# Performance work log

Measured on AMD Instinct MI355X. Metric: run time of the kernel, lower is better.

## Reference

```python
import jax, jax.numpy as jnp
import numpy as np

LAMBDA_COLOR = 0.01
BLUR = 0.01          # geomloss blur
P = 2                # geomloss p
EPS_FINAL = BLUR ** P  # 1e-4
# Note: with scaling=1.2 (>1), geomloss's epsilon_schedule arange is empty, so
# eps_list = [diameter**p, blur**p] -> exactly two annealing stages.


def cost_matrix(x, y, lambda_color):
    # x: [B,N,6], y: [B,M,6]
    cx, col_x = x[..., :3], x[..., 3:]
    cy, col_y = y[..., :3], y[..., 3:]
    max_norm = jnp.max(jnp.linalg.norm(jnp.concatenate([cx, cy], axis=1), axis=-1))
    s = 1.0 / (max_norm + 1e-6)
    cxn, cyn = cx * s, cy * s
    coord = jnp.sum((cxn[:, :, None, :] - cyn[:, None, :, :]) ** 2, axis=-1)  # [B,N,M]
    col_x = jnp.clip(col_x, 0.0, 1.0)
    col_y = jnp.clip(col_y, 0.0, 1.0)
    col = jnp.sum((col_x[:, :, None, :] - col_y[:, None, :, :]) ** 2, axis=-1)
    return jnp.maximum(coord + lambda_color * col, 0.0)


def softmin(eps, C, h):
    # h: [B,M] = log_weights + potential/eps ; C: [B,N,M]
    return -eps * jax.nn.logsumexp(h[:, None, :] - C / eps, axis=2)  # [B,N]


def sinkhorn_distance(x, y, lambda_color):
    B, N, _ = x.shape
    M = y.shape[1]
    a_log = jnp.full((B, N), -np.log(N), dtype=x.dtype)
    b_log = jnp.full((B, M), -np.log(M), dtype=x.dtype)

    C_xy = cost_matrix(x, y, lambda_color)          # [B,N,M]
    C_yx = jnp.swapaxes(C_xy, 1, 2)                 # cost is symmetric in x<->y

    # diameter over raw 6-d features (geomloss max_diameter)
    pts = jnp.concatenate([x.reshape(-1, x.shape[-1]), y.reshape(-1, y.shape[-1])], axis=0)
    diameter = jnp.linalg.norm(pts.max(0) - pts.min(0))
    eps_list = (diameter ** P, jnp.asarray(EPS_FINAL, x.dtype))

    # Sinkhorn loop runs without gradient through the potentials (geomloss semantics)
    Cs_xy = jax.lax.stop_gradient(C_xy)
    Cs_yx = jax.lax.stop_gradient(C_yx)

    eps = eps_list[0]
    f = softmin(eps, Cs_xy, b_log)   # potential on x
    g = softmin(eps, Cs_yx, a_log)   # potential on y
    for eps in eps_list:
        ft = softmin(eps, Cs_xy, b_log + g / eps)
        gt = softmin(eps, Cs_yx, a_log + f / eps)
        f, g = 0.5 * (f + ft), 0.5 * (g + gt)

    # final extrapolation with gradient-carrying cost, detached dual potentials
    eps = eps_list[-1]
    f_new = softmin(eps, C_xy, b_log + jax.lax.stop_gradient(g) / eps)
    g_new = softmin(eps, C_yx, a_log + jax.lax.stop_gradient(f) / eps)

    # <a,f> + <b,g> with uniform weights
    ot = f_new.mean(axis=1) + g_new.mean(axis=1)   # [B]
    return ot.mean() * 10.0


def setup_inputs() -> dict:
    key = jax.random.key(0)
    kx, ky = jax.random.split(key)
    x = jax.random.normal(kx, (4, 4096, 6), dtype=jnp.float32)
    y = jax.random.normal(ky, (4, 4096, 6), dtype=jnp.float32)
    return {"x": x, "y": y}


def reference(x, y):
    return sinkhorn_distance(x, y, LAMBDA_COLOR)
```

## Files before the change

### kernel.cpp

```cpp
#include <hip/hip_runtime.h>

#define B_ 4
#define N_ 4096
#define ROWS (B_ * N_)
#define PTS_TOTAL (2 * ROWS)

#define LOG2E 1.4426950408889634f
#define LN2   0.6931471805599453f
#define EPS1  1e-4f
#define NEG_LOG2M (-12.0f)
#define EPS1LNM 8.317766166719343e-4f
#define ENC_STRIDE 32

typedef _Float16 h2 __attribute__((ext_vector_type(2)));
typedef _Float16 v8h __attribute__((ext_vector_type(8)));
typedef float f32x4 __attribute__((ext_vector_type(4)));

__device__ inline float fexp2(float x) { return __builtin_amdgcn_exp2f(x); }
__device__ inline float flog2(float x) { return __builtin_amdgcn_logf(x); }

__device__ inline unsigned fenc(float f) {
  unsigned u = __float_as_uint(f);
  return (u & 0x80000000u) ? ~u : (u | 0x80000000u);
}
__device__ inline float fdec(unsigned u) {
  return (u & 0x80000000u) ? __uint_as_float(u & 0x7fffffffu)
                           : __uint_as_float(~u);
}
__device__ inline unsigned pkh2(float a, float b) {
  h2 hv; hv.x = (_Float16)a; hv.y = (_Float16)b;
  return __builtin_bit_cast(unsigned, hv);
}
__device__ inline v8h bcv8(uint4 u) { return __builtin_bit_cast(v8h, u); }

__global__ void init_kernel(unsigned* enc, float* MOM) {
  int t = threadIdx.x;
  if (t < 13) enc[t * ENC_STRIDE] = 0u;
  if (t < 512) MOM[t] = 0.0f;
}

__global__ __launch_bounds__(256) void reduce_kernel(
    const float* __restrict__ x, const float* __restrict__ y,
    unsigned* __restrict__ enc) {
  int idx = blockIdx.x * 256 + threadIdx.x;
  bool isx = idx < ROWS;
  const float* p = (isx ? x : y) + (size_t)(isx ? idx : idx - ROWS) * 6;
  float d[6];
#pragma unroll
  for (int k = 0; k < 6; ++k) d[k] = p[k];
  unsigned e[13];
  e[0] = fenc(d[0] * d[0] + d[1] * d[1] + d[2] * d[2]);
#pragma unroll
  for (int k = 0; k < 6; ++k) {
    e[1 + k] = fenc(d[k]);
    e[7 + k] = fenc(-d[k]);
  }
#pragma unroll
  for (int off = 32; off > 0; off >>= 1) {
#pragma unroll
    for (int k = 0; k < 13; ++k) {
      unsigned o = (unsigned)__shfl_xor((int)e[k], off);
      e[k] = e[k] > o ? e[k] : o;
    }
  }
  __shared__ unsigned sh[4][13];
  int wave = threadIdx.x >> 6, lane = threadIdx.x & 63;
  if (lane == 0) {
#pragma unroll
    for (int k = 0; k < 13; ++k) sh[wave][k] = e[k];
  }
  __syncthreads();
  if (threadIdx.x < 13) {
    unsigned v = sh[0][threadIdx.x];
#pragma unroll
    for (int w = 1; w < 4; ++w) v = v > sh[w][threadIdx.x] ? v : sh[w][threadIdx.x];
    atomicMax(&enc[threadIdx.x * ENC_STRIDE], v);
  }
}

__global__ __launch_bounds__(256) void pack_kernel(
    const float* __restrict__ x, const float* __restrict__ y,
    float4* __restrict__ XP, uint4* __restrict__ AREC,
    uint4* __restrict__ BREC, const unsigned* __restrict__ enc,
    float* __restrict__ sc, float* __restrict__ MOM1) {
  int g = blockIdx.x * 256 + threadIdx.x;
  int side = g >> 14, local = g & (ROWS - 1), batch = local >> 12;
  float s = 1.0f / (sqrtf(fdec(enc[0])) + 1e-6f);
  float eps0 = 0.0f;
#pragma unroll
  for (int k = 0; k < 6; ++k) {
    float dd = fdec(enc[(1 + k) * ENC_STRIDE]) + fdec(enc[(7 + k) * ENC_STRIDE]);
    eps0 += dd * dd;
  }
  if (g == 0) sc[0] = eps0;

  const float* p = (side ? y : x) + (size_t)local * 6;
  float v[6];
  v[0] = p[0] * s; v[1] = p[1] * s; v[2] = p[2] * s;
  v[3] = 0.1f * fminf(fmaxf(p[3], 0.0f), 1.0f);
  v[4] = 0.1f * fminf(fmaxf(p[4], 0.0f), 1.0f);
  v[5] = 0.1f * fminf(fmaxf(p[5], 0.0f), 1.0f);
  float q = v[0]*v[0] + v[1]*v[1] + v[2]*v[2] + v[3]*v[3] + v[4]*v[4] + v[5]*v[5];
  XP[(size_t)g * 2]     = make_float4(v[0], v[1], v[2], v[3]);
  XP[(size_t)g * 2 + 1] = make_float4(v[4], v[5], q, 0.0f);
  unsigned w01 = pkh2(v[0], v[1]), w23 = pkh2(v[2], v[3]), w45 = pkh2(v[4], v[5]);
  AREC[g] = (uint4){w01, w23, w45, pkh2(1.0f, 0.0f)};
  BREC[g] = (uint4){w01, w23, w45, 0u};

  float w = fexp2(NEG_LOG2M - q * (LOG2E / eps0));
  float acc[28];
  acc[0] = w;
  int kk = 1;
#pragma unroll
  for (int d = 0; d < 6; ++d) acc[kk++] = w * v[d];
#pragma unroll
  for (int d = 0; d < 6; ++d) {
    float wv = w * v[d];
#pragma unroll
    for (int e = d; e < 6; ++e) acc[kk++] = wv * v[e];
  }
#pragma unroll
  for (int off = 32; off > 0; off >>= 1) {
#pragma unroll
    for (int k = 0; k < 28; ++k) acc[k] += __shfl_xor(acc[k], off);
  }
  __shared__ float sh[4][28];
  int wave = threadIdx.x >> 6, lane = threadIdx.x & 63;
  if (lane == 0) {
#pragma unroll
    for (int k = 0; k < 28; ++k) sh[wave][k] = acc[k];
  }
  __syncthreads();
  if (threadIdx.x < 28) {
    float vv = (sh[0][threadIdx.x] + sh[1][threadIdx.x]) +
               (sh[2][threadIdx.x] + sh[3][threadIdx.x]);
    atomicAdd(&MOM1[(side * 4 + batch) * 32 + threadIdx.x], vv);
  }
}

__device__ inline float taylor_f(const float* __restrict__ M, const float* v,
                                 float q, float eps0) {
  float sc2 = 2.0f * LOG2E / eps0;
  float p[6];
#pragma unroll
  for (int d = 0; d < 6; ++d) p[d] = v[d] * sc2;
  float t1 = 0.0f;
#pragma unroll
  for (int d = 0; d < 6; ++d) t1 += p[d] * M[1 + d];
  float t2 = 0.0f;
  int kk = 7;
#pragma unroll
  for (int d = 0; d < 6; ++d) {
#pragma unroll
    for (int e = d; e < 6; ++e) {
      float coef = (d == e) ? 1.0f : 2.0f;
      t2 += coef * p[d] * p[e] * M[kk];
      kk++;
    }
  }
  float S = M[0] + LN2 * t1 + (0.5f * LN2 * LN2) * t2;
  return q - eps0 * LN2 * flog2(S);
}

__global__ __launch_bounds__(256) void rows1_kernel(
    const float4* __restrict__ XP, const float* __restrict__ MOM1,
    float* __restrict__ MOM2, float* __restrict__ FG1,
    const float* __restrict__ sc) {
  int g = blockIdx.x * 256 + threadIdx.x;
  int side = g >> 14, local = g & (ROWS - 1), batch = local >> 12;
  float eps0 = sc[0];
  float4 a = XP[(size_t)g * 2], b = XP[(size_t)g * 2 + 1];
  float v[6] = {a.x, a.y, a.z, a.w, b.x, b.y};
  float q = b.z;
  const float* M = MOM1 + (((side ^ 1) * 4 + batch) * 32);
  float f1 = taylor_f(M, v, q, eps0);
  FG1[g] = f1;
  float w = fexp2(NEG_LOG2M + (f1 - q) * (LOG2E / eps0));
  float acc[28];
  acc[0] = w;
  int kk = 1;
#pragma unroll
  for (int d = 0; d < 6; ++d) acc[kk++] = w * v[d];
#pragma unroll
  for (int d = 0; d < 6; ++d) {
    float wv = w * v[d];
#pragma unroll
    for (int e = d; e < 6; ++e) acc[kk++] = wv * v[e];
  }
#pragma unroll
  for (int off = 32; off > 0; off >>= 1) {
#pragma unroll
    for (int k = 0; k < 28; ++k) acc[k] += __shfl_xor(acc[k], off);
  }
  __shared__ float sh[4][28];
  int wave = threadIdx.x >> 6, lane = threadIdx.x & 63;
  if (lane == 0) {
#pragma unroll
    for (int k = 0; k < 28; ++k) sh[wave][k] = acc[k];
  }
  __syncthreads();
  if (threadIdx.x < 28) {
    float vv = (sh[0][threadIdx.x] + sh[1][threadIdx.x]) +
               (sh[2][threadIdx.x] + sh[3][threadIdx.x]);
    atomicAdd(&MOM2[(side * 4 + batch) * 32 + threadIdx.x], vv);
  }
}

__global__ __launch_bounds__(256) void rows2_kernel(
    const float4* __restrict__ XP, const float* __restrict__ MOM2,
    const float* __restrict__ FG1, float* __restrict__ FG2,
    unsigned* __restrict__ BRECu, const float* __restrict__ sc) {
  int g = blockIdx.x * 256 + threadIdx.x;
  int side = g >> 14, local = g & (ROWS - 1), batch = local >> 12;
  float eps0 = sc[0];
  float4 a = XP[(size_t)g * 2], b = XP[(size_t)g * 2 + 1];
  float v[6] = {a.x, a.y, a.z, a.w, b.x, b.y};
  float q = b.z;
  const float* M = MOM2 + (((side ^ 1) * 4 + batch) * 32);
  float f_t = taylor_f(M, v, q, eps0);
  float f2v = 0.5f * (FG1[g] + f_t);
  FG2[g] = f2v;
  float hs2 = 0.5f * (f2v - q - EPS1LNM);
  BRECu[4 * g + 3] = pkh2(hs2, 0.0f);
}

__global__ __launch_bounds__(256) void softmax_pair_kernel(
    const uint4* __restrict__ AREC, const uint4* __restrict__ BIN,
    uint4* __restrict__ BOUT, const float* __restrict__ XPf,
    const float* __restrict__ prev, float* __restrict__ part) {
  int t = threadIdx.x;
  int wave = t >> 6, lane = t & 63;
  int l16 = lane & 15;
  bool ld = lane < 16;
  int grow0 = blockIdx.x * 32;
  int side = grow0 >> 14;
  int batch = (grow0 & (ROWS - 1)) >> 12;
  int colrec0 = (side ^ 1) * ROWS + batch * 4096 + wave * 1024;

  uint4 z4 = (uint4){0u, 0u, 0u, 0u};
  uint4 a1u = z4, a2u = z4;
  if (ld) {
    a1u = AREC[grow0 + l16];
    a2u = AREC[grow0 + 16 + l16];
  }
  v8h a1 = bcv8(a1u), a2 = bcv8(a2u);

  f32x4 m2a = {-3.0e38f, -3.0e38f, -3.0e38f, -3.0e38f};
  f32x4 m2b = m2a;
  const f32x4 cz = {0.0f, 0.0f, 0.0f, 0.0f};

#pragma unroll 4
  for (int tt = 0; tt < 64; ++tt) {
    uint4 bu = z4;
    if (ld) bu = BIN[colrec0 + tt * 16 + l16];
    v8h b = bcv8(bu);
    f32x4 d1 = __builtin_amdgcn_mfma_f32_16x16x32_f16(a1, b, cz, 0, 0, 0);
    f32x4 d2 = __builtin_amdgcn_mfma_f32_16x16x32_f16(a2, b, cz, 0, 0, 0);
    m2a = __builtin_elementwise_max(m2a, d1);
    m2b = __builtin_elementwise_max(m2b, d2);
  }

#pragma unroll
  for (int off = 1; off <= 8; off <<= 1) {
#pragma unroll
    for (int r = 0; r < 4; ++r) {
      m2a[r] = fmaxf(m2a[r], __shfl_xor(m2a[r], off));
      m2b[r] = fmaxf(m2b[r], __shfl_xor(m2b[r], off));
    }
  }

  __shared__ float lm[4][32];
  __shared__ float fsh[32];
  if (l16 == 0) {
    int qd = lane >> 4;
#pragma unroll
    for (int r = 0; r < 4; ++r) {
      lm[wave][qd * 4 + r] = m2a[r];
      lm[wave][16 + qd * 4 + r] = m2b[r];
    }
  }
  __syncthreads();
  if (t < 32) {
    int g = grow0 + t;
    float m = fmaxf(fmaxf(lm[0][t], lm[1][t]), fmaxf(lm[2][t], lm[3][t]));
    float q = XPf[(size_t)g * 8 + 6];
    float f_t = q - 2.0f * m;
    float fo = prev ? 0.5f * (prev[g] + f_t) : f_t;
    if (BOUT) {
      float hs = 0.5f * (fo - q - EPS1LNM);
      uint4 ar = AREC[g];
      BOUT[g] = (uint4){ar.x, ar.y, ar.z, pkh2(hs, 0.0f)};
    }
    if (part) {
      fsh[t] = fo;
      __builtin_amdgcn_s_waitcnt(0);
      if (t == 0) {
        float ssum = 0.0f;
#pragma unroll
        for (int k = 0; k < 32; ++k) ssum += fsh[k];
        part[blockIdx.x] = ssum;
      }
    }
  }
}

__global__ __launch_bounds__(256) void final_kernel(
    const float* __restrict__ part, float* __restrict__ out) {
  float acc = 0.0f;
  for (int i = threadIdx.x; i < 1024; i += 256) acc += part[i];
  __shared__ float sh[256];
  sh[threadIdx.x] = acc;
  __syncthreads();
  for (int st = 128; st > 0; st >>= 1) {
    if (threadIdx.x < st) sh[threadIdx.x] += sh[threadIdx.x + st];
    __syncthreads();
  }
  if (threadIdx.x == 0) out[0] = sh[0] * (10.0f / (float)ROWS);
}

extern "C" void kernel_launch(void* const* d_in, const int* in_sizes, int n_in,
                              void* d_out, int out_size, void* d_ws,
                              size_t ws_size, hipStream_t stream) {
  const float* x = (const float*)d_in[0];
  const float* y = (const float*)d_in[1];
  float* out = (float*)d_out;
  float* w = (float*)d_ws;
  unsigned* enc = (unsigned*)d_ws;
  float* sc   = w + 448;
  float* MOM  = w + 512;
  float* MOM1 = MOM;
  float* MOM2 = MOM + 256;
  float* base = w + 1024;
  float4* XP   = (float4*)base;
  uint4* AREC  = (uint4*)(base + 262144);
  uint4* BRECA = (uint4*)(base + 262144 + 131072);
  uint4* BRECB = (uint4*)(base + 262144 + 262144);
  float* FG1   = base + 262144 + 262144 + 131072;
  float* FG2   = FG1 + PTS_TOTAL;
  float* PART  = FG2 + PTS_TOTAL;

  init_kernel<<<1, 512, 0, stream>>>(enc, MOM);
  reduce_kernel<<<PTS_TOTAL / 256, 256, 0, stream>>>(x, y, enc);
  pack_kernel<<<PTS_TOTAL / 256, 256, 0, stream>>>(x, y, XP, AREC, BRECA, enc,
                                                   sc, MOM1);
  rows1_kernel<<<PTS_TOTAL / 256, 256, 0, stream>>>(XP, MOM1, MOM2, FG1, sc);
  rows2_kernel<<<PTS_TOTAL / 256, 256, 0, stream>>>(XP, MOM2, FG1, FG2,
                                                    (unsigned*)BRECA, sc);
  softmax_pair_kernel<<<1024, 256, 0, stream>>>(AREC, BRECA, BRECB,
                                                (const float*)XP, FG2, nullptr);
  softmax_pair_kernel<<<1024, 256, 0, stream>>>(AREC, BRECB, nullptr,
                                                (const float*)XP, nullptr, PART);
  final_kernel<<<1, 256, 0, stream>>>(PART, out);
}
```

Measured before the change: 118.0 us.

## Fuse all stages into one cooperative persistent kernel with grid syncs

Replaces the chain of eight kernel launches with a single cooperative kernel of 512 blocks that separates stages with grid-wide syncs. Per-point values stay in registers between the moment stages instead of going through global memory. Each block now handles 64 rows in the MFMA max stage, so every loaded B tile is reused across four A fragments. The cost is grid-sync barriers, only 128 of 512 blocks doing work in the early stages, and a host-side occupancy query on every call, with the old multi-kernel path kept as a fallback.

```diff
diff --git a/kernel.cpp b/kernel.cpp
--- a/kernel.cpp
+++ b/kernel.cpp
@@ -1,13 +1,13 @@
 #include <hip/hip_runtime.h>
-
-#define B_ 4
-#define N_ 4096
-#define ROWS (B_ * N_)
-#define PTS_TOTAL (2 * ROWS)
+#include <hip/hip_cooperative_groups.h>
+
+namespace cg = cooperative_groups;
+
+#define ROWS 16384
+#define PTS_TOTAL 32768
 
 #define LOG2E 1.4426950408889634f
 #define LN2   0.6931471805599453f
-#define EPS1  1e-4f
 #define NEG_LOG2M (-12.0f)
 #define EPS1LNM 8.317766166719343e-4f
 #define ENC_STRIDE 32
@@ -32,6 +32,272 @@
   return __builtin_bit_cast(unsigned, hv);
 }
 __device__ inline v8h bcv8(uint4 u) { return __builtin_bit_cast(v8h, u); }
+
+__device__ inline float taylor_f(const float* __restrict__ M, const float* v,
+                                 float q, float eps0) {
+  float sc2 = 2.0f * LOG2E / eps0;
+  float p[6];
+#pragma unroll
+  for (int d = 0; d < 6; ++d) p[d] = v[d] * sc2;
+  float t1 = 0.0f;
+#pragma unroll
+  for (int d = 0; d < 6; ++d) t1 += p[d] * M[1 + d];
+  float t2 = 0.0f;
+  int kk = 7;
+#pragma unroll
+  for (int d = 0; d < 6; ++d) {
+#pragma unroll
+    for (int e = d; e < 6; ++e) {
+      float coef = (d == e) ? 1.0f : 2.0f;
+      t2 += coef * p[d] * p[e] * M[kk];
+      kk++;
+    }
+  }
+  float S = M[0] + LN2 * t1 + (0.5f * LN2 * LN2) * t2;
+  return q - eps0 * LN2 * flog2(S);
+}
+
+__device__ inline void mom_acc(float w, const float* v, float* acc) {
+  acc[0] = w;
+  int kk = 1;
+#pragma unroll
+  for (int d = 0; d < 6; ++d) acc[kk++] = w * v[d];
+#pragma unroll
+  for (int d = 0; d < 6; ++d) {
+    float wv = w * v[d];
+#pragma unroll
+    for (int e = d; e < 6; ++e) acc[kk++] = wv * v[e];
+  }
+}
+
+__global__ __launch_bounds__(256, 2) void mega_kernel(
+    const float* __restrict__ x, const float* __restrict__ y,
+    float* __restrict__ out, unsigned* __restrict__ enc,
+    float* __restrict__ MOM, uint4* __restrict__ AREC,
+    uint4* __restrict__ BRECA, uint4* __restrict__ BRECB,
+    float* __restrict__ Q, float* __restrict__ FG2,
+    float* __restrict__ PART) {
+  cg::grid_group grid = cg::this_grid();
+  const int t = threadIdx.x;
+  const int blk = blockIdx.x;
+  const int gtid = blk * 256 + t;
+  const int wave = t >> 6, lane = t & 63;
+  float* MOM1 = MOM;
+  float* MOM2 = MOM + 256;
+
+  __shared__ unsigned shu[4][13];
+  __shared__ float shm[4][28];
+  __shared__ float lm[4][64];
+  __shared__ float fsh[64];
+  __shared__ float red[256];
+
+  if (gtid < 13) enc[gtid * ENC_STRIDE] = 0u;
+  if (gtid < 512) MOM[gtid] = 0.0f;
+  grid.sync();
+
+  if (blk < 128) {
+    bool isx = gtid < ROWS;
+    const float* p = (isx ? x : y) + (size_t)(isx ? gtid : gtid - ROWS) * 6;
+    float d[6];
+#pragma unroll
+    for (int k = 0; k < 6; ++k) d[k] = p[k];
+    unsigned e[13];
+    e[0] = fenc(d[0] * d[0] + d[1] * d[1] + d[2] * d[2]);
+#pragma unroll
+    for (int k = 0; k < 6; ++k) {
+      e[1 + k] = fenc(d[k]);
+      e[7 + k] = fenc(-d[k]);
+    }
+#pragma unroll
+    for (int off = 32; off > 0; off >>= 1) {
+#pragma unroll
+      for (int k = 0; k < 13; ++k) {
+        unsigned o = (unsigned)__shfl_xor((int)e[k], off);
+        e[k] = e[k] > o ? e[k] : o;
+      }
+    }
+    if (lane == 0) {
+#pragma unroll
+      for (int k = 0; k < 13; ++k) shu[wave][k] = e[k];
+    }
+    __syncthreads();
+    if (t < 13) {
+      unsigned v2 = shu[0][t];
+#pragma unroll
+      for (int w = 1; w < 4; ++w) v2 = v2 > shu[w][t] ? v2 : shu[w][t];
+      atomicMax(&enc[t * ENC_STRIDE], v2);
+    }
+  }
+  grid.sync();
+
+  float v[6] = {0, 0, 0, 0, 0, 0};
+  float q = 0.0f, eps0 = 1.0f, f1 = 0.0f;
+  int side = gtid >> 14, batch = (gtid & (ROWS - 1)) >> 12;
+
+  if (blk < 128) {
+    float s = 1.0f / (sqrtf(fdec(enc[0])) + 1e-6f);
+    eps0 = 0.0f;
+#pragma unroll
+    for (int k = 0; k < 6; ++k) {
+      float dd = fdec(enc[(1 + k) * ENC_STRIDE]) +
+                 fdec(enc[(7 + k) * ENC_STRIDE]);
+      eps0 += dd * dd;
+    }
+    int local = gtid & (ROWS - 1);
+    const float* p = (side ? y : x) + (size_t)local * 6;
+    v[0] = p[0] * s; v[1] = p[1] * s; v[2] = p[2] * s;
+    v[3] = 0.1f * fminf(fmaxf(p[3], 0.0f), 1.0f);
+    v[4] = 0.1f * fminf(fmaxf(p[4], 0.0f), 1.0f);
+    v[5] = 0.1f * fminf(fmaxf(p[5], 0.0f), 1.0f);
+    q = v[0]*v[0] + v[1]*v[1] + v[2]*v[2] + v[3]*v[3] + v[4]*v[4] + v[5]*v[5];
+    Q[gtid] = q;
+    unsigned w01 = pkh2(v[0], v[1]), w23 = pkh2(v[2], v[3]),
+             w45 = pkh2(v[4], v[5]);
+    AREC[gtid]  = (uint4){w01, w23, w45, pkh2(1.0f, 0.0f)};
+    BRECA[gtid] = (uint4){w01, w23, w45, 0u};
+
+    float acc[28];
+    mom_acc(fexp2(NEG_LOG2M - q * (LOG2E / eps0)), v, acc);
+#pragma unroll
+    for (int off = 32; off > 0; off >>= 1) {
+#pragma unroll
+      for (int k = 0; k < 28; ++k) acc[k] += __shfl_xor(acc[k], off);
+    }
+    if (lane == 0) {
+#pragma unroll
+      for (int k = 0; k < 28; ++k) shm[wave][k] = acc[k];
+    }
+    __syncthreads();
+    if (t < 28) {
+      float vv = (shm[0][t] + shm[1][t]) + (shm[2][t] + shm[3][t]);
+      atomicAdd(&MOM1[(side * 4 + batch) * 32 + t], vv);
+    }
+  }
+  grid.sync();
+
+  if (blk < 128) {
+    const float* M = MOM1 + (((side ^ 1) * 4 + batch) * 32);
+    f1 = taylor_f(M, v, q, eps0);
+    float acc[28];
+    mom_acc(fexp2(NEG_LOG2M + (f1 - q) * (LOG2E / eps0)), v, acc);
+#pragma unroll
+    for (int off = 32; off > 0; off >>= 1) {
+#pragma unroll
+      for (int k = 0; k < 28; ++k) acc[k] += __shfl_xor(acc[k], off);
+    }
+    if (lane == 0) {
+#pragma unroll
+      for (int k = 0; k < 28; ++k) shm[wave][k] = acc[k];
+    }
+    __syncthreads();
+    if (t < 28) {
+      float vv = (shm[0][t] + shm[1][t]) + (shm[2][t] + shm[3][t]);
+      atomicAdd(&MOM2[(side * 4 + batch) * 32 + t], vv);
+    }
+  }
+  grid.sync();
+
+  if (blk < 128) {
+    const float* M = MOM2 + (((side ^ 1) * 4 + batch) * 32);
+    float f_t = taylor_f(M, v, q, eps0);
+    float f2v = 0.5f * (f1 + f_t);
+    FG2[gtid] = f2v;
+    ((unsigned*)BRECA)[4 * gtid + 3] = pkh2(0.5f * (f2v - q - EPS1LNM), 0.0f);
+  }
+  grid.sync();
+
+  const int grow0 = blk * 64;
+  const int mside = grow0 >> 14;
+  const int mbatch = (grow0 & (ROWS - 1)) >> 12;
+  const int colrec0 = (mside ^ 1) * ROWS + mbatch * 4096 + wave * 1024;
+  const int l16 = lane & 15;
+  const bool ld = lane < 16;
+  const uint4 z4 = (uint4){0u, 0u, 0u, 0u};
+  v8h a[4];
+#pragma unroll
+  for (int i = 0; i < 4; ++i) {
+    uint4 au = z4;
+    if (ld) au = AREC[grow0 + i * 16 + l16];
+    a[i] = bcv8(au);
+  }
+  const f32x4 cz = {0.0f, 0.0f, 0.0f, 0.0f};
+
+#pragma unroll
+  for (int phase = 0; phase < 2; ++phase) {
+    const uint4* __restrict__ BIN = (phase == 0) ? BRECA : BRECB;
+    f32x4 m2[4];
+#pragma unroll
+    for (int i = 0; i < 4; ++i)
+      m2[i] = (f32x4){-3.0e38f, -3.0e38f, -3.0e38f, -3.0e38f};
+#pragma unroll 4
+    for (int tt = 0; tt < 64; ++tt) {
+      uint4 bu = z4;
+      if (ld) bu = BIN[colrec0 + tt * 16 + l16];
+      v8h b = bcv8(bu);
+#pragma unroll
+      for (int i = 0; i < 4; ++i) {
+        f32x4 d = __builtin_amdgcn_mfma_f32_16x16x32_f16(a[i], b, cz, 0, 0, 0);
+        m2[i] = __builtin_elementwise_max(m2[i], d);
+      }
+    }
+#pragma unroll
+    for (int off = 1; off <= 8; off <<= 1) {
+#pragma unroll
+      for (int i = 0; i < 4; ++i) {
+#pragma unroll
+        for (int r = 0; r < 4; ++r)
+          m2[i][r] = fmaxf(m2[i][r], __shfl_xor(m2[i][r], off));
+      }
+    }
+    if (l16 == 0) {
+      int qd = lane >> 4;
+#pragma unroll
+      for (int i = 0; i < 4; ++i) {
+#pragma unroll
+        for (int r = 0; r < 4; ++r) lm[wave][i * 16 + qd * 4 + r] = m2[i][r];
+      }
+    }
+    __syncthreads();
+    if (phase == 0) {
+      if (t < 64) {
+        int g = grow0 + t;
+        float m = fmaxf(fmaxf(lm[0][t], lm[1][t]), fmaxf(lm[2][t], lm[3][t]));
+        float qq = Q[g];
+        float fo = 0.5f * (FG2[g] + (qq - 2.0f * m));
+        uint4 ar = AREC[g];
+        BRECB[g] = (uint4){ar.x, ar.y, ar.z,
+                           pkh2(0.5f * (fo - qq - EPS1LNM), 0.0f)};
+      }
+      grid.sync();
+    } else {
+      if (t < 64) {
+        int g = grow0 + t;
+        float m = fmaxf(fmaxf(lm[0][t], lm[1][t]), fmaxf(lm[2][t], lm[3][t]));
+        fsh[t] = Q[g] - 2.0f * m;
+      }
+      __syncthreads();
+      if (t == 0) {
+        float ssum = 0.0f;
+#pragma unroll
+        for (int k = 0; k < 64; ++k) ssum += fsh[k];
+        PART[blk] = ssum;
+      }
+      grid.sync();
+    }
+  }
+
+  if (blk == 0) {
+    float acc = (t < 512 - 256) ? PART[256 + t] : 0.0f;
+    acc += PART[t];
+    red[t] = acc;
+    __syncthreads();
+    for (int st = 128; st > 0; st >>= 1) {
+      if (t < st) red[t] += red[t + st];
+      __syncthreads();
+    }
+    if (t == 0) out[0] = red[0] * (10.0f / (float)ROWS);
+  }
+}
 
 __global__ void init_kernel(unsigned* enc, float* MOM) {
   int t = threadIdx.x;
@@ -73,14 +339,15 @@
   if (threadIdx.x < 13) {
     unsigned v = sh[0][threadIdx.x];
 #pragma unroll
-    for (int w = 1; w < 4; ++w) v = v > sh[w][threadIdx.x] ? v : sh[w][threadIdx.x];
+    for (int w = 1; w < 4; ++w)
+      v = v > sh[w][threadIdx.x] ? v : sh[w][threadIdx.x];
     atomicMax(&enc[threadIdx.x * ENC_STRIDE], v);
   }
 }
 
 __global__ __launch_bounds__(256) void pack_kernel(
     const float* __restrict__ x, const float* __restrict__ y,
-    float4* __restrict__ XP, uint4* __restrict__ AREC,
+    float* __restrict__ Q, float* __restrict__ V6, uint4* __restrict__ AREC,
     uint4* __restrict__ BREC, const unsigned* __restrict__ enc,
     float* __restrict__ sc, float* __restrict__ MOM1) {
   int g = blockIdx.x * 256 + threadIdx.x;
@@ -93,7 +360,6 @@
     eps0 += dd * dd;
   }
   if (g == 0) sc[0] = eps0;
-
   const float* p = (side ? y : x) + (size_t)local * 6;
   float v[6];
   v[0] = p[0] * s; v[1] = p[1] * s; v[2] = p[2] * s;
@@ -101,24 +367,16 @@
   v[4] = 0.1f * fminf(fmaxf(p[4], 0.0f), 1.0f);
   v[5] = 0.1f * fminf(fmaxf(p[5], 0.0f), 1.0f);
   float q = v[0]*v[0] + v[1]*v[1] + v[2]*v[2] + v[3]*v[3] + v[4]*v[4] + v[5]*v[5];
-  XP[(size_t)g * 2]     = make_float4(v[0], v[1], v[2], v[3]);
-  XP[(size_t)g * 2 + 1] = make_float4(v[4], v[5], q, 0.0f);
-  unsigned w01 = pkh2(v[0], v[1]), w23 = pkh2(v[2], v[3]), w45 = pkh2(v[4], v[5]);
+  Q[g] = q;
+#pragma unroll
+  for (int d = 0; d < 6; ++d) V6[(size_t)g * 6 + d] = v[d];
+  unsigned w01 = pkh2(v[0], v[1]), w23 = pkh2(v[2], v[3]),
+           w45 = pkh2(v[4], v[5]);
   AREC[g] = (uint4){w01, w23, w45, pkh2(1.0f, 0.0f)};
   BREC[g] = (uint4){w01, w23, w45, 0u};
 
-  float w = fexp2(NEG_LOG2M - q * (LOG2E / eps0));
   float acc[28];
-  acc[0] = w;
-  int kk = 1;
-#pragma unroll
-  for (int d = 0; d < 6; ++d) acc[kk++] = w * v[d];
-#pragma unroll
-  for (int d = 0; d < 6; ++d) {
-    float wv = w * v[d];
-#pragma unroll
-    for (int e = d; e < 6; ++e) acc[kk++] = wv * v[e];
-  }
+  mom_acc(fexp2(NEG_LOG2M - q * (LOG2E / eps0)), v, acc);
 #pragma unroll
   for (int off = 32; off > 0; off >>= 1) {
 #pragma unroll
@@ -138,55 +396,22 @@
   }
 }
 
-__device__ inline float taylor_f(const float* __restrict__ M, const float* v,
-                                 float q, float eps0) {
-  float sc2 = 2.0f * LOG2E / eps0;
-  float p[6];
-#pragma unroll
-  for (int d = 0; d < 6; ++d) p[d] = v[d] * sc2;
-  float t1 = 0.0f;
-#pragma unroll
-  for (int d = 0; d < 6; ++d) t1 += p[d] * M[1 + d];
-  float t2 = 0.0f;
-  int kk = 7;
-#pragma unroll
-  for (int d = 0; d < 6; ++d) {
-#pragma unroll
-    for (int e = d; e < 6; ++e) {
-      float coef = (d == e) ? 1.0f : 2.0f;
-      t2 += coef * p[d] * p[e] * M[kk];
-      kk++;
-    }
-  }
-  float S = M[0] + LN2 * t1 + (0.5f * LN2 * LN2) * t2;
-  return q - eps0 * LN2 * flog2(S);
-}
-
 __global__ __launch_bounds__(256) void rows1_kernel(
-    const float4* __restrict__ XP, const float* __restrict__ MOM1,
-    float* __restrict__ MOM2, float* __restrict__ FG1,
-    const float* __restrict__ sc) {
+    const float* __restrict__ Q, const float* __restrict__ V6,
+    const float* __restrict__ MOM1, float* __restrict__ MOM2,
+    float* __restrict__ FG1, const float* __restrict__ sc) {
   int g = blockIdx.x * 256 + threadIdx.x;
   int side = g >> 14, local = g & (ROWS - 1), batch = local >> 12;
   float eps0 = sc[0];
-  float4 a = XP[(size_t)g * 2], b = XP[(size_t)g * 2 + 1];
-  float v[6] = {a.x, a.y, a.z, a.w, b.x, b.y};
-  float q = b.z;
+  float v[6];
+#pragma unroll
+  for (int d = 0; d < 6; ++d) v[d] = V6[(size_t)g * 6 + d];
+  float q = Q[g];
   const float* M = MOM1 + (((side ^ 1) * 4 + batch) * 32);
   float f1 = taylor_f(M, v, q, eps0);
   FG1[g] = f1;
-  float w = fexp2(NEG_LOG2M + (f1 - q) * (LOG2E / eps0));
   float acc[28];
-  acc[0] = w;
-  int kk = 1;
-#pragma unroll
-  for (int d = 0; d < 6; ++d) acc[kk++] = w * v[d];
-#pragma unroll
-  for (int d = 0; d < 6; ++d) {
-    float wv = w * v[d];
-#pragma unroll
-    for (int e = d; e < 6; ++e) acc[kk++] = wv * v[e];
-  }
+  mom_acc(fexp2(NEG_LOG2M + (f1 - q) * (LOG2E / eps0)), v, acc);
 #pragma unroll
   for (int off = 32; off > 0; off >>= 1) {
 #pragma unroll
@@ -207,26 +432,27 @@
 }
 
 __global__ __launch_bounds__(256) void rows2_kernel(
-    const float4* __restrict__ XP, const float* __restrict__ MOM2,
-    const float* __restrict__ FG1, float* __restrict__ FG2,
-    unsigned* __restrict__ BRECu, const float* __restrict__ sc) {
+    const float* __restrict__ Q, const float* __restrict__ V6,
+    const float* __restrict__ MOM2, const float* __restrict__ FG1,
+    float* __restrict__ FG2, unsigned* __restrict__ BRECu,
+    const float* __restrict__ sc) {
   int g = blockIdx.x * 256 + threadIdx.x;
   int side = g >> 14, local = g & (ROWS - 1), batch = local >> 12;
   float eps0 = sc[0];
-  float4 a = XP[(size_t)g * 2], b = XP[(size_t)g * 2 + 1];
-  float v[6] = {a.x, a.y, a.z, a.w, b.x, b.y};
-  float q = b.z;
+  float v[6];
+#pragma unroll
+  for (int d = 0; d < 6; ++d) v[d] = V6[(size_t)g * 6 + d];
+  float q = Q[g];
   const float* M = MOM2 + (((side ^ 1) * 4 + batch) * 32);
   float f_t = taylor_f(M, v, q, eps0);
   float f2v = 0.5f * (FG1[g] + f_t);
   FG2[g] = f2v;
-  float hs2 = 0.5f * (f2v - q - EPS1LNM);
-  BRECu[4 * g + 3] = pkh2(hs2, 0.0f);
+  BRECu[4 * g + 3] = pkh2(0.5f * (f2v - q - EPS1LNM), 0.0f);
 }
 
 __global__ __launch_bounds__(256) void softmax_pair_kernel(
     const uint4* __restrict__ AREC, const uint4* __restrict__ BIN,
-    uint4* __restrict__ BOUT, const float* __restrict__ XPf,
+    uint4* __restrict__ BOUT, const float* __restrict__ Q,
     const float* __restrict__ prev, float* __restrict__ part) {
   int t = threadIdx.x;
   int wave = t >> 6, lane = t & 63;
@@ -236,7 +462,6 @@
   int side = grow0 >> 14;
   int batch = (grow0 & (ROWS - 1)) >> 12;
   int colrec0 = (side ^ 1) * ROWS + batch * 4096 + wave * 1024;
-
   uint4 z4 = (uint4){0u, 0u, 0u, 0u};
   uint4 a1u = z4, a2u = z4;
   if (ld) {
@@ -244,11 +469,9 @@
     a2u = AREC[grow0 + 16 + l16];
   }
   v8h a1 = bcv8(a1u), a2 = bcv8(a2u);
-
   f32x4 m2a = {-3.0e38f, -3.0e38f, -3.0e38f, -3.0e38f};
   f32x4 m2b = m2a;
   const f32x4 cz = {0.0f, 0.0f, 0.0f, 0.0f};
-
 #pragma unroll 4
   for (int tt = 0; tt < 64; ++tt) {
     uint4 bu = z4;
@@ -259,7 +482,6 @@
     m2a = __builtin_elementwise_max(m2a, d1);
     m2b = __builtin_elementwise_max(m2b, d2);
   }
-
 #pragma unroll
   for (int off = 1; off <= 8; off <<= 1) {
 #pragma unroll
@@ -268,7 +490,6 @@
       m2b[r] = fmaxf(m2b[r], __shfl_xor(m2b[r], off));
     }
   }
-
   __shared__ float lm[4][32];
   __shared__ float fsh[32];
   if (l16 == 0) {
@@ -283,31 +504,29 @@
   if (t < 32) {
     int g = grow0 + t;
     float m = fmaxf(fmaxf(lm[0][t], lm[1][t]), fmaxf(lm[2][t], lm[3][t]));
-    float q = XPf[(size_t)g * 8 + 6];
+    float q = Q[g];
     float f_t = q - 2.0f * m;
     float fo = prev ? 0.5f * (prev[g] + f_t) : f_t;
     if (BOUT) {
-      float hs = 0.5f * (fo - q - EPS1LNM);
       uint4 ar = AREC[g];
-      BOUT[g] = (uint4){ar.x, ar.y, ar.z, pkh2(hs, 0.0f)};
-    }
-    if (part) {
-      fsh[t] = fo;
-      __builtin_amdgcn_s_waitcnt(0);
-      if (t == 0) {
-        float ssum = 0.0f;
-#pragma unroll
-        for (int k = 0; k < 32; ++k) ssum += fsh[k];
-        part[blockIdx.x] = ssum;
-      }
-    }
+      BOUT[g] = (uint4){ar.x, ar.y, ar.z,
+                        pkh2(0.5f * (fo - q - EPS1LNM), 0.0f)};
+    }
+    if (part) fsh[t] = fo;
+  }
+  __syncthreads();
+  if (part && t == 0) {
+    float ssum = 0.0f;
+#pragma unroll
+    for (int k = 0; k < 32; ++k) ssum += fsh[k];
+    part[blockIdx.x] = ssum;
   }
 }
 
 __global__ __launch_bounds__(256) void final_kernel(
-    const float* __restrict__ part, float* __restrict__ out) {
+    const float* __restrict__ part, int n, float* __restrict__ out) {
   float acc = 0.0f;
-  for (int i = threadIdx.x; i < 1024; i += 256) acc += part[i];
+  for (int i = threadIdx.x; i < n; i += 256) acc += part[i];
   __shared__ float sh[256];
   sh[threadIdx.x] = acc;
   __syncthreads();
@@ -326,29 +545,52 @@
   float* out = (float*)d_out;
   float* w = (float*)d_ws;
   unsigned* enc = (unsigned*)d_ws;
-  float* sc   = w + 448;
-  float* MOM  = w + 512;
+  float* sc  = w + 448;
+  float* MOM = w + 512;
   float* MOM1 = MOM;
   float* MOM2 = MOM + 256;
   float* base = w + 1024;
-  float4* XP   = (float4*)base;
-  uint4* AREC  = (uint4*)(base + 262144);
-  uint4* BRECA = (uint4*)(base + 262144 + 131072);
-  uint4* BRECB = (uint4*)(base + 262144 + 262144);
-  float* FG1   = base + 262144 + 262144 + 131072;
-  float* FG2   = FG1 + PTS_TOTAL;
-  float* PART  = FG2 + PTS_TOTAL;
-
-  init_kernel<<<1, 512, 0, stream>>>(enc, MOM);
-  reduce_kernel<<<PTS_TOTAL / 256, 256, 0, stream>>>(x, y, enc);
-  pack_kernel<<<PTS_TOTAL / 256, 256, 0, stream>>>(x, y, XP, AREC, BRECA, enc,
-                                                   sc, MOM1);
-  rows1_kernel<<<PTS_TOTAL / 256, 256, 0, stream>>>(XP, MOM1, MOM2, FG1, sc);
-  rows2_kernel<<<PTS_TOTAL / 256, 256, 0, stream>>>(XP, MOM2, FG1, FG2,
-                                                    (unsigned*)BRECA, sc);
-  softmax_pair_kernel<<<1024, 256, 0, stream>>>(AREC, BRECA, BRECB,
-                                                (const float*)XP, FG2, nullptr);
-  softmax_pair_kernel<<<1024, 256, 0, stream>>>(AREC, BRECB, nullptr,
-                                                (const float*)XP, nullptr, PART);
-  final_kernel<<<1, 256, 0, stream>>>(PART, out);
-}
+  uint4* AREC  = (uint4*)base;
+  uint4* BRECA = (uint4*)(base + 131072);
+  uint4* BRECB = (uint4*)(base + 262144);
+  float* Q    = base + 393216;
+  float* V6   = Q + PTS_TOTAL;
+  float* FG1  = V6 + 6 * PTS_TOTAL;
+  float* FG2  = FG1 + PTS_TOTAL;
+  float* PART = FG2 + PTS_TOTAL;
+
+  int capacity = 0;
+  {
+    int nb = 0;
+    if (hipOccupancyMaxActiveBlocksPerMultiprocessor(
+            &nb, (const void*)mega_kernel, 256, 0) == hipSuccess) {
+      hipDeviceProp_t prop;
+      int dev = 0;
+      hipGetDevice(&dev);
+      if (hipGetDeviceProperties(&prop, dev) == hipSuccess)
+        capacity = nb * prop.multiProcessorCount;
+    }
+  }
+
+  if (capacity >= 512) {
+    void* args[] = {(void*)&x,    (void*)&y,     (void*)&out,   (void*)&enc,
+                    (void*)&MOM,  (void*)&AREC,  (void*)&BRECA, (void*)&BRECB,
+                    (void*)&Q,    (void*)&FG2,   (void*)&PART};
+    hipLaunchCooperativeKernel((const void*)mega_kernel, dim3(512), dim3(256),
+                               args, 0, stream);
+  } else {
+    init_kernel<<<1, 512, 0, stream>>>(enc, MOM);
+    reduce_kernel<<<PTS_TOTAL / 256, 256, 0, stream>>>(x, y, enc);
+    pack_kernel<<<PTS_TOTAL / 256, 256, 0, stream>>>(x, y, Q, V6, AREC, BRECA,
+                                                     enc, sc, MOM1);
+    rows1_kernel<<<PTS_TOTAL / 256, 256, 0, stream>>>(Q, V6, MOM1, MOM2, FG1,
+                                                      sc);
+    rows2_kernel<<<PTS_TOTAL / 256, 256, 0, stream>>>(Q, V6, MOM2, FG1, FG2,
+                                                      (unsigned*)BRECA, sc);
+    softmax_pair_kernel<<<1024, 256, 0, stream>>>(AREC, BRECA, BRECB, Q, FG2,
+                                                  nullptr);
+    softmax_pair_kernel<<<1024, 256, 0, stream>>>(AREC, BRECB, nullptr, Q,
+                                                  nullptr, PART);
+    final_kernel<<<1, 256, 0, stream>>>(PART, 1024, out);
+  }
+}
```

Result: slower. 464.7 us (+293.9%).
